# Kernel tuning notes

Hardware: AMD Instinct MI355X
Metric: run time of the kernel (lower is better)

The kernel has to match this reference:

```python
import jax, jax.numpy as jnp
import numpy as np

B, LQ, LA, H = 32, 1024, 1024, 512
NEG_INF = jnp.float32(-1e7)  # matches torch masked_fill_(-10000000.0)


def setup_inputs() -> dict:
    key = jax.random.key(0)
    k1, k2, k3, k4 = jax.random.split(key, 4)
    q = jax.random.normal(k1, (B, LQ, H), dtype=jnp.float32)
    a = jax.random.normal(k2, (B, LA, H), dtype=jnp.float32)
    q_mask = jax.random.randint(k3, (B, LQ, 1), 0, 2).astype(jnp.int32)
    a_mask = jax.random.randint(k4, (B, LA, 1), 0, 2).astype(jnp.int32)
    # learned scalar, initialized exactly as in __init__
    temperature = jnp.float32(1.0 / np.sqrt(H))
    return {"q": q, "a": a, "q_mask": q_mask, "a_mask": a_mask,
            "temperature": temperature}


def reference(q, a, q_mask, a_mask, temperature):
    # scaled co-attention scores: [B, Lq, La]
    attn = jnp.einsum('bqh,bah->bqa', q, a) * temperature
    # validity mask via outer product of per-token masks (nonzero = valid)
    mask = jnp.matmul(q_mask.astype(jnp.float32),
                      a_mask.transpose(0, 2, 1).astype(jnp.float32)) != 0
    attn = jnp.where(mask, attn, NEG_INF)
    # dual-axis softmax over the SAME score matrix
    attn_q = jax.nn.softmax(attn, axis=1)  # normalize over Lq
    attn_a = jax.nn.softmax(attn, axis=2)  # normalize over La
    # aggregation: a_s = attn_q^T @ q -> [B, La, H]; q_s = attn_a @ a -> [B, Lq, H]
    a_s = jnp.einsum('bqa,bqh->bah', attn_q, q)
    q_s = jnp.einsum('bqa,bah->bqh', attn_a, a)
    return (jnp.concatenate([q, q_s], axis=-1),
            jnp.concatenate([a, a_s], axis=-1))
```

## Files before the change

### kernel.cpp

```cpp
#include <hip/hip_runtime.h>
#include <cstdint>
#include <cstddef>

#define NB   32
#define LQA  1024
#define HD   512

typedef __attribute__((ext_vector_type(4))) float  f32x4;
typedef __attribute__((ext_vector_type(8))) short  s16x8;
typedef __attribute__((ext_vector_type(4))) unsigned short u16x4;

static __device__ __forceinline__ unsigned short f2bf(float f) {
  unsigned int u = __builtin_bit_cast(unsigned int, f);
  u += 0x7fffu + ((u >> 16) & 1u);
  return (unsigned short)(u >> 16);
}
static __device__ __forceinline__ float bf2f(unsigned short h) {
  unsigned int u = ((unsigned int)h) << 16;
  return __builtin_bit_cast(float, u);
}
static __device__ __forceinline__ u16x4 cvt4(f32x4 v) {
  u16x4 r;
  r.x = f2bf(v.x); r.y = f2bf(v.y); r.z = f2bf(v.z); r.w = f2bf(v.w);
  return r;
}

__global__ __launch_bounds__(256) void k_transpose_copy(
    const float* __restrict__ src,
    float* __restrict__ out_left,
    unsigned short* __restrict__ dstT)
{
  const int b  = blockIdx.z;
  const int h0 = blockIdx.x * 64;
  const int q0 = blockIdx.y * 64;
  const int t  = threadIdx.x;

  __shared__ unsigned short T[64 * 68];

  const float* sb = src + (size_t)b * LQA * HD;
  float* ob       = out_left + (size_t)b * LQA * 1024;
  unsigned short* db = dstT + (size_t)b * HD * LQA;

#pragma unroll
  for (int j = 0; j < 4; ++j) {
    int f = t + 256 * j;
    int r = f >> 4;
    int c = (f & 15) * 4;
    f32x4 v = *(const f32x4*)(sb + (size_t)(q0 + r) * HD + h0 + c);
    *(f32x4*)(ob + (size_t)(q0 + r) * 1024 + h0 + c) = v;
    *(u16x4*)&T[r * 68 + c] = cvt4(v);
  }
  __syncthreads();
#pragma unroll
  for (int j = 0; j < 4; ++j) {
    int f = t + 256 * j;
    int orow = f >> 4;
    int c = (f & 15) * 4;
    u16x4 v;
    v.x = T[(c + 0) * 68 + orow];
    v.y = T[(c + 1) * 68 + orow];
    v.z = T[(c + 2) * 68 + orow];
    v.w = T[(c + 3) * 68 + orow];
    *(u16x4*)&db[(size_t)(h0 + orow) * LQA + q0 + c] = v;
  }
}

__global__ __launch_bounds__(256) void k_scores(
    const float* __restrict__ q, const float* __restrict__ a,
    const int* __restrict__ qmask, const int* __restrict__ amask,
    const float* __restrict__ temp_p,
    unsigned short* __restrict__ E, unsigned short* __restrict__ ET)
{
  const int b  = blockIdx.z;
  const int m0 = blockIdx.x * 128;
  const int n0 = blockIdx.y * 128;
  const int t  = threadIdx.x;
  const int lane = t & 63;
  const int w  = t >> 6;
  const int moff = (w & 1) * 64;
  const int noff = (w >> 1) * 64;
  const int lrow = lane & 15;
  const int quad = lane >> 4;

  __shared__ unsigned short As[128 * 32];
  __shared__ unsigned short Bs[128 * 32];
  __shared__ unsigned short Cs[128 * 132];

  const float* qb = q + (size_t)b * LQA * HD;
  const float* ab = a + (size_t)b * LQA * HD;

  f32x4 acc[4][4];
#pragma unroll
  for (int i = 0; i < 4; ++i)
#pragma unroll
    for (int j = 0; j < 4; ++j) acc[i][j] = (f32x4)0.f;

  for (int kt = 0; kt < HD / 32; ++kt) {
#pragma unroll
    for (int j = 0; j < 4; ++j) {
      int f = t + 256 * j;
      int row = f >> 3;
      int ch  = f & 7;
      f32x4 va = *(const f32x4*)(qb + (size_t)(m0 + row) * HD + kt * 32 + ch * 4);
      f32x4 vb = *(const f32x4*)(ab + (size_t)(n0 + row) * HD + kt * 32 + ch * 4);
      *(u16x4*)&As[row * 32 + ch * 4] = cvt4(va);
      *(u16x4*)&Bs[row * 32 + ch * 4] = cvt4(vb);
    }
    __syncthreads();
    s16x8 af[4], bfr[4];
#pragma unroll
    for (int i = 0; i < 4; ++i) {
      af[i]  = *(const s16x8*)&As[(moff + i * 16 + lrow) * 32 + quad * 8];
      bfr[i] = *(const s16x8*)&Bs[(noff + i * 16 + lrow) * 32 + quad * 8];
    }
#pragma unroll
    for (int i = 0; i < 4; ++i)
#pragma unroll
      for (int j = 0; j < 4; ++j)
        acc[i][j] = __builtin_amdgcn_mfma_f32_16x16x32_bf16(af[i], bfr[j], acc[i][j], 0, 0, 0);
    __syncthreads();
  }

  const float temp = temp_p[0];
  const int* qmb = qmask + b * LQA;
  const int* amb = amask + b * LQA;
#pragma unroll
  for (int i = 0; i < 4; ++i) {
#pragma unroll
    for (int j = 0; j < 4; ++j) {
      int ncol = noff + j * 16 + lrow;
      float am = (amb[n0 + ncol] != 0) ? 1.f : 0.f;
#pragma unroll
      for (int r = 0; r < 4; ++r) {
        int mrow = moff + i * 16 + quad * 4 + r;
        float qm = (qmb[m0 + mrow] != 0) ? 1.f : 0.f;
        float e = __expf(acc[i][j][r] * temp) * am * qm;
        Cs[mrow * 132 + ncol] = f2bf(e);
      }
    }
  }
  __syncthreads();
  const size_t Ebase = (size_t)b * LQA * LQA;
#pragma unroll
  for (int jj = 0; jj < 16; ++jj) {
    int f = t + 256 * jj;
    int row = f >> 5;
    int c = (f & 31) * 4;
    u16x4 v = *(const u16x4*)&Cs[row * 132 + c];
    *(u16x4*)&E[Ebase + (size_t)(m0 + row) * LQA + n0 + c] = v;
  }
#pragma unroll
  for (int jj = 0; jj < 16; ++jj) {
    int f = t + 256 * jj;
    int orow = f >> 5;
    int c = (f & 31) * 4;
    u16x4 v;
    v.x = Cs[(c + 0) * 132 + orow];
    v.y = Cs[(c + 1) * 132 + orow];
    v.z = Cs[(c + 2) * 132 + orow];
    v.w = Cs[(c + 3) * 132 + orow];
    *(u16x4*)&ET[Ebase + (size_t)(n0 + orow) * LQA + m0 + c] = v;
  }
}

__global__ __launch_bounds__(256) void k_rowsum(
    const unsigned short* __restrict__ Emat, float2* __restrict__ invadd)
{
  const int t = threadIdx.x;
  const int rowg = blockIdx.x * 16 + (t >> 4);
  const int s = t & 15;
  const unsigned short* rp = Emat + (size_t)rowg * LQA;
  float sum = 0.f;
#pragma unroll
  for (int it = 0; it < 16; ++it) {
    u16x4 v = *(const u16x4*)&rp[it * 64 + s * 4];
    sum += bf2f(v.x) + bf2f(v.y) + bf2f(v.z) + bf2f(v.w);
  }
  sum += __shfl_xor(sum, 1);
  sum += __shfl_xor(sum, 2);
  sum += __shfl_xor(sum, 4);
  sum += __shfl_xor(sum, 8);
  if (s == 0) {
    float2 o;
    if (sum > 0.f) { o.x = 1.f / sum; o.y = 0.f; }
    else           { o.x = 0.f;       o.y = 1.f / 1024.f; }
    invadd[rowg] = o;
  }
}

__global__ __launch_bounds__(256) void k_agg(
    const unsigned short* __restrict__ Emat,
    const unsigned short* __restrict__ Bt,
    const float2* __restrict__ invadd,
    float* __restrict__ outp)
{
  const int b  = blockIdx.z;
  const int m0 = blockIdx.x * 128;
  const int n0 = blockIdx.y * 128;
  const int t  = threadIdx.x;
  const int lane = t & 63;
  const int w  = t >> 6;
  const int moff = (w & 1) * 64;
  const int noff = (w >> 1) * 64;
  const int lrow = lane & 15;
  const int quad = lane >> 4;

  __shared__ unsigned short As[128 * 32];
  __shared__ unsigned short Bs[128 * 32];

  const unsigned short* Eb = Emat + (size_t)b * LQA * LQA;
  const unsigned short* Bb = Bt + (size_t)b * HD * LQA;
  const float2* ia = invadd + b * LQA;

  float inv_r[4], add_r[4];
#pragma unroll
  for (int j = 0; j < 4; ++j) {
    int row = (t >> 3) + 32 * j;
    float2 v = ia[m0 + row];
    inv_r[j] = v.x; add_r[j] = v.y;
  }

  f32x4 acc[4][4];
#pragma unroll
  for (int i = 0; i < 4; ++i)
#pragma unroll
    for (int j = 0; j < 4; ++j) acc[i][j] = (f32x4)0.f;

  for (int kt = 0; kt < LQA / 32; ++kt) {
#pragma unroll
    for (int j = 0; j < 4; ++j) {
      int f = t + 256 * j;
      int row = f >> 3;
      int ch  = f & 7;
      u16x4 ev = *(const u16x4*)&Eb[(size_t)(m0 + row) * LQA + kt * 32 + ch * 4];
      f32x4 p;
      p.x = bf2f(ev.x) * inv_r[j] + add_r[j];
      p.y = bf2f(ev.y) * inv_r[j] + add_r[j];
      p.z = bf2f(ev.z) * inv_r[j] + add_r[j];
      p.w = bf2f(ev.w) * inv_r[j] + add_r[j];
      *(u16x4*)&As[row * 32 + ch * 4] = cvt4(p);
      u16x4 bv = *(const u16x4*)&Bb[(size_t)(n0 + row) * LQA + kt * 32 + ch * 4];
      *(u16x4*)&Bs[row * 32 + ch * 4] = bv;
    }
    __syncthreads();
    s16x8 af[4], bfr[4];
#pragma unroll
    for (int i = 0; i < 4; ++i) {
      af[i]  = *(const s16x8*)&As[(moff + i * 16 + lrow) * 32 + quad * 8];
      bfr[i] = *(const s16x8*)&Bs[(noff + i * 16 + lrow) * 32 + quad * 8];
    }
#pragma unroll
    for (int i = 0; i < 4; ++i)
#pragma unroll
      for (int j = 0; j < 4; ++j)
        acc[i][j] = __builtin_amdgcn_mfma_f32_16x16x32_bf16(af[i], bfr[j], acc[i][j], 0, 0, 0);
    __syncthreads();
  }

#pragma unroll
  for (int i = 0; i < 4; ++i) {
#pragma unroll
    for (int j = 0; j < 4; ++j) {
      int ncol = noff + j * 16 + lrow;
#pragma unroll
      for (int r = 0; r < 4; ++r) {
        int mrow = moff + i * 16 + quad * 4 + r;
        outp[(size_t)b * LQA * 1024 + (size_t)(m0 + mrow) * 1024 + 512 + n0 + ncol] =
            acc[i][j][r];
      }
    }
  }
}

extern "C" void kernel_launch(void* const* d_in, const int* in_sizes, int n_in,
                              void* d_out, int out_size, void* d_ws, size_t ws_size,
                              hipStream_t stream) {
  const float* q    = (const float*)d_in[0];
  const float* a    = (const float*)d_in[1];
  const int*   qm   = (const int*)d_in[2];
  const int*   am   = (const int*)d_in[3];
  const float* temp = (const float*)d_in[4];

  float* out0 = (float*)d_out;
  float* out1 = out0 + (size_t)NB * LQA * 1024;

  char* ws = (char*)d_ws;
  const size_t MB = 1024ull * 1024ull;
  unsigned short* E    = (unsigned short*)(ws);
  unsigned short* ET   = (unsigned short*)(ws + 64 * MB);
  unsigned short* qT   = (unsigned short*)(ws + 128 * MB);
  unsigned short* aT   = (unsigned short*)(ws + 160 * MB);
  float2* invq = (float2*)(ws + 192 * MB);
  float2* inva = (float2*)(ws + 192 * MB + 262144);

  k_transpose_copy<<<dim3(8, 16, NB), 256, 0, stream>>>(q, out0, qT);
  k_transpose_copy<<<dim3(8, 16, NB), 256, 0, stream>>>(a, out1, aT);
  k_scores<<<dim3(8, 8, NB), 256, 0, stream>>>(q, a, qm, am, temp, E, ET);
  k_rowsum<<<dim3(NB * LQA / 16), 256, 0, stream>>>(E, invq);
  k_rowsum<<<dim3(NB * LQA / 16), 256, 0, stream>>>(ET, inva);
  k_agg<<<dim3(8, 4, NB), 256, 0, stream>>>(E,  aT, invq, out0);
  k_agg<<<dim3(8, 4, NB), 256, 0, stream>>>(ET, qT, inva, out1);
}
```

Before: 679.2 us.

## Use direct global-to-LDS loads with precomputed bf16 inputs and deferred normalization

```diff
diff --git a/kernel.cpp b/kernel.cpp
--- a/kernel.cpp
+++ b/kernel.cpp
@@ -25,10 +25,17 @@
   return r;
 }
 
+typedef __attribute__((address_space(1))) const void gas_void;
+typedef __attribute__((address_space(3))) void las_void;
+static __device__ __forceinline__ void gload_lds16(const void* g, void* l) {
+  __builtin_amdgcn_global_load_lds((gas_void*)g, (las_void*)l, 16, 0, 0);
+}
+
 __global__ __launch_bounds__(256) void k_transpose_copy(
     const float* __restrict__ src,
     float* __restrict__ out_left,
-    unsigned short* __restrict__ dstT)
+    unsigned short* __restrict__ dstT,
+    unsigned short* __restrict__ dstN)
 {
   const int b  = blockIdx.z;
   const int h0 = blockIdx.x * 64;
@@ -39,7 +46,8 @@
 
   const float* sb = src + (size_t)b * LQA * HD;
   float* ob       = out_left + (size_t)b * LQA * 1024;
-  unsigned short* db = dstT + (size_t)b * HD * LQA;
+  unsigned short* db  = dstT + (size_t)b * HD * LQA;
+  unsigned short* dbn = dstN + (size_t)b * LQA * HD;
 
 #pragma unroll
   for (int j = 0; j < 4; ++j) {
@@ -48,7 +56,9 @@
     int c = (f & 15) * 4;
     f32x4 v = *(const f32x4*)(sb + (size_t)(q0 + r) * HD + h0 + c);
     *(f32x4*)(ob + (size_t)(q0 + r) * 1024 + h0 + c) = v;
-    *(u16x4*)&T[r * 68 + c] = cvt4(v);
+    u16x4 cv = cvt4(v);
+    *(u16x4*)&dbn[(size_t)(q0 + r) * HD + h0 + c] = cv;
+    *(u16x4*)&T[r * 68 + c] = cv;
   }
   __syncthreads();
 #pragma unroll
@@ -66,7 +76,7 @@
 }
 
 __global__ __launch_bounds__(256) void k_scores(
-    const float* __restrict__ q, const float* __restrict__ a,
+    const unsigned short* __restrict__ qb16, const unsigned short* __restrict__ ab16,
     const int* __restrict__ qmask, const int* __restrict__ amask,
     const float* __restrict__ temp_p,
     unsigned short* __restrict__ E, unsigned short* __restrict__ ET)
@@ -82,12 +92,22 @@
   const int lrow = lane & 15;
   const int quad = lane >> 4;
 
-  __shared__ unsigned short As[128 * 32];
-  __shared__ unsigned short Bs[128 * 32];
-  __shared__ unsigned short Cs[128 * 132];
-
-  const float* qb = q + (size_t)b * LQA * HD;
-  const float* ab = a + (size_t)b * LQA * HD;
+  __shared__ __align__(16) unsigned short smem[128 * 132];
+  unsigned short* As = smem;
+  unsigned short* Bs = smem + 4096;
+
+  const unsigned short* qb = qb16 + (size_t)b * LQA * HD;
+  const unsigned short* ab = ab16 + (size_t)b * LQA * HD;
+
+  const int fa = t, fb = t + 256;
+  const unsigned short* qg0 = qb + (size_t)(m0 + (fa >> 2)) * HD + (fa & 3) * 8;
+  const unsigned short* qg1 = qb + (size_t)(m0 + (fb >> 2)) * HD + (fb & 3) * 8;
+  const unsigned short* ag0 = ab + (size_t)(n0 + (fa >> 2)) * HD + (fa & 3) * 8;
+  const unsigned short* ag1 = ab + (size_t)(n0 + (fb >> 2)) * HD + (fb & 3) * 8;
+  unsigned short* As0 = As + w * 512;
+  unsigned short* As1 = As + (4 + w) * 512;
+  unsigned short* Bs0 = Bs + w * 512;
+  unsigned short* Bs1 = Bs + (4 + w) * 512;
 
   f32x4 acc[4][4];
 #pragma unroll
@@ -96,16 +116,11 @@
     for (int j = 0; j < 4; ++j) acc[i][j] = (f32x4)0.f;
 
   for (int kt = 0; kt < HD / 32; ++kt) {
-#pragma unroll
-    for (int j = 0; j < 4; ++j) {
-      int f = t + 256 * j;
-      int row = f >> 3;
-      int ch  = f & 7;
-      f32x4 va = *(const f32x4*)(qb + (size_t)(m0 + row) * HD + kt * 32 + ch * 4);
-      f32x4 vb = *(const f32x4*)(ab + (size_t)(n0 + row) * HD + kt * 32 + ch * 4);
-      *(u16x4*)&As[row * 32 + ch * 4] = cvt4(va);
-      *(u16x4*)&Bs[row * 32 + ch * 4] = cvt4(vb);
-    }
+    const int ko = kt * 32;
+    gload_lds16(qg0 + ko, As0);
+    gload_lds16(qg1 + ko, As1);
+    gload_lds16(ag0 + ko, Bs0);
+    gload_lds16(ag1 + ko, Bs1);
     __syncthreads();
     s16x8 af[4], bfr[4];
 #pragma unroll
@@ -121,6 +136,7 @@
     __syncthreads();
   }
 
+  unsigned short* Cs = smem;
   const float temp = temp_p[0];
   const int* qmb = qmask + b * LQA;
   const int* amb = amask + b * LQA;
@@ -163,7 +179,7 @@
   }
 }
 
-__global__ __launch_bounds__(256) void k_rowsum(
+__global__ __launch_bounds__(256) void k_rowsum_stats(
     const unsigned short* __restrict__ Emat, float2* __restrict__ invadd)
 {
   const int t = threadIdx.x;
@@ -188,10 +204,31 @@
   }
 }
 
+__global__ __launch_bounds__(256) void k_rowsum_plain(
+    const unsigned short* __restrict__ M, float* __restrict__ sums)
+{
+  const int t = threadIdx.x;
+  const int rowg = blockIdx.x * 16 + (t >> 4);
+  const int s = t & 15;
+  const unsigned short* rp = M + (size_t)rowg * LQA;
+  float sum = 0.f;
+#pragma unroll
+  for (int it = 0; it < 16; ++it) {
+    u16x4 v = *(const u16x4*)&rp[it * 64 + s * 4];
+    sum += bf2f(v.x) + bf2f(v.y) + bf2f(v.z) + bf2f(v.w);
+  }
+  sum += __shfl_xor(sum, 1);
+  sum += __shfl_xor(sum, 2);
+  sum += __shfl_xor(sum, 4);
+  sum += __shfl_xor(sum, 8);
+  if (s == 0) sums[rowg] = sum;
+}
+
 __global__ __launch_bounds__(256) void k_agg(
     const unsigned short* __restrict__ Emat,
     const unsigned short* __restrict__ Bt,
     const float2* __restrict__ invadd,
+    const float* __restrict__ bsum,
     float* __restrict__ outp)
 {
   const int b  = blockIdx.z;
@@ -205,20 +242,21 @@
   const int lrow = lane & 15;
   const int quad = lane >> 4;
 
-  __shared__ unsigned short As[128 * 32];
-  __shared__ unsigned short Bs[128 * 32];
+  __shared__ __align__(16) unsigned short As[128 * 32];
+  __shared__ __align__(16) unsigned short Bs[128 * 32];
 
   const unsigned short* Eb = Emat + (size_t)b * LQA * LQA;
   const unsigned short* Bb = Bt + (size_t)b * HD * LQA;
-  const float2* ia = invadd + b * LQA;
-
-  float inv_r[4], add_r[4];
-#pragma unroll
-  for (int j = 0; j < 4; ++j) {
-    int row = (t >> 3) + 32 * j;
-    float2 v = ia[m0 + row];
-    inv_r[j] = v.x; add_r[j] = v.y;
-  }
+
+  const int fa = t, fb = t + 256;
+  const unsigned short* eg0 = Eb + (size_t)(m0 + (fa >> 2)) * LQA + (fa & 3) * 8;
+  const unsigned short* eg1 = Eb + (size_t)(m0 + (fb >> 2)) * LQA + (fb & 3) * 8;
+  const unsigned short* bg0 = Bb + (size_t)(n0 + (fa >> 2)) * LQA + (fa & 3) * 8;
+  const unsigned short* bg1 = Bb + (size_t)(n0 + (fb >> 2)) * LQA + (fb & 3) * 8;
+  unsigned short* As0 = As + w * 512;
+  unsigned short* As1 = As + (4 + w) * 512;
+  unsigned short* Bs0 = Bs + w * 512;
+  unsigned short* Bs1 = Bs + (4 + w) * 512;
 
   f32x4 acc[4][4];
 #pragma unroll
@@ -227,21 +265,11 @@
     for (int j = 0; j < 4; ++j) acc[i][j] = (f32x4)0.f;
 
   for (int kt = 0; kt < LQA / 32; ++kt) {
-#pragma unroll
-    for (int j = 0; j < 4; ++j) {
-      int f = t + 256 * j;
-      int row = f >> 3;
-      int ch  = f & 7;
-      u16x4 ev = *(const u16x4*)&Eb[(size_t)(m0 + row) * LQA + kt * 32 + ch * 4];
-      f32x4 p;
-      p.x = bf2f(ev.x) * inv_r[j] + add_r[j];
-      p.y = bf2f(ev.y) * inv_r[j] + add_r[j];
-      p.z = bf2f(ev.z) * inv_r[j] + add_r[j];
-      p.w = bf2f(ev.w) * inv_r[j] + add_r[j];
-      *(u16x4*)&As[row * 32 + ch * 4] = cvt4(p);
-      u16x4 bv = *(const u16x4*)&Bb[(size_t)(n0 + row) * LQA + kt * 32 + ch * 4];
-      *(u16x4*)&Bs[row * 32 + ch * 4] = bv;
-    }
+    const int ko = kt * 32;
+    gload_lds16(eg0 + ko, As0);
+    gload_lds16(eg1 + ko, As1);
+    gload_lds16(bg0 + ko, Bs0);
+    gload_lds16(bg1 + ko, Bs1);
     __syncthreads();
     s16x8 af[4], bfr[4];
 #pragma unroll
@@ -257,16 +285,21 @@
     __syncthreads();
   }
 
+  const float2* ia = invadd + b * LQA;
+  const float* bs = bsum + b * HD;
+  float* ob = outp + (size_t)b * LQA * 1024;
 #pragma unroll
   for (int i = 0; i < 4; ++i) {
 #pragma unroll
     for (int j = 0; j < 4; ++j) {
       int ncol = noff + j * 16 + lrow;
+      float bsv = bs[n0 + ncol];
 #pragma unroll
       for (int r = 0; r < 4; ++r) {
         int mrow = moff + i * 16 + quad * 4 + r;
-        outp[(size_t)b * LQA * 1024 + (size_t)(m0 + mrow) * 1024 + 512 + n0 + ncol] =
-            acc[i][j][r];
+        float2 v = ia[m0 + mrow];
+        ob[(size_t)(m0 + mrow) * 1024 + 512 + n0 + ncol] =
+            v.x * acc[i][j][r] + v.y * bsv;
       }
     }
   }
@@ -275,6 +308,7 @@
 extern "C" void kernel_launch(void* const* d_in, const int* in_sizes, int n_in,
                               void* d_out, int out_size, void* d_ws, size_t ws_size,
                               hipStream_t stream) {
+  (void)in_sizes; (void)n_in; (void)out_size; (void)ws_size;
   const float* q    = (const float*)d_in[0];
   const float* a    = (const float*)d_in[1];
   const int*   qm   = (const int*)d_in[2];
@@ -290,14 +324,20 @@
   unsigned short* ET   = (unsigned short*)(ws + 64 * MB);
   unsigned short* qT   = (unsigned short*)(ws + 128 * MB);
   unsigned short* aT   = (unsigned short*)(ws + 160 * MB);
-  float2* invq = (float2*)(ws + 192 * MB);
-  float2* inva = (float2*)(ws + 192 * MB + 262144);
-
-  k_transpose_copy<<<dim3(8, 16, NB), 256, 0, stream>>>(q, out0, qT);
-  k_transpose_copy<<<dim3(8, 16, NB), 256, 0, stream>>>(a, out1, aT);
-  k_scores<<<dim3(8, 8, NB), 256, 0, stream>>>(q, a, qm, am, temp, E, ET);
-  k_rowsum<<<dim3(NB * LQA / 16), 256, 0, stream>>>(E, invq);
-  k_rowsum<<<dim3(NB * LQA / 16), 256, 0, stream>>>(ET, inva);
-  k_agg<<<dim3(8, 4, NB), 256, 0, stream>>>(E,  aT, invq, out0);
-  k_agg<<<dim3(8, 4, NB), 256, 0, stream>>>(ET, qT, inva, out1);
-}
+  unsigned short* qb16 = (unsigned short*)(ws + 192 * MB);
+  unsigned short* ab16 = (unsigned short*)(ws + 224 * MB);
+  float2* invq = (float2*)(ws + 256 * MB);
+  float2* inva = (float2*)(ws + 256 * MB + 262144);
+  float*  qsum = (float*)(ws + 256 * MB + 524288);
+  float*  asum = (float*)(ws + 256 * MB + 524288 + 65536);
+
+  k_transpose_copy<<<dim3(8, 16, NB), 256, 0, stream>>>(q, out0, qT, qb16);
+  k_transpose_copy<<<dim3(8, 16, NB), 256, 0, stream>>>(a, out1, aT, ab16);
+  k_rowsum_plain<<<dim3(NB * HD / 16), 256, 0, stream>>>(qT, qsum);
+  k_rowsum_plain<<<dim3(NB * HD / 16), 256, 0, stream>>>(aT, asum);
+  k_scores<<<dim3(8, 8, NB), 256, 0, stream>>>(qb16, ab16, qm, am, temp, E, ET);
+  k_rowsum_stats<<<dim3(NB * LQA / 16), 256, 0, stream>>>(E, invq);
+  k_rowsum_stats<<<dim3(NB * LQA / 16), 256, 0, stream>>>(ET, inva);
+  k_agg<<<dim3(8, 4, NB), 256, 0, stream>>>(E,  aT, invq, asum, out0);
+  k_agg<<<dim3(8, 4, NB), 256, 0, stream>>>(ET, qT, inva, qsum, out1);
+}
```

Result: faster. 628.2 us (-7.5%).
